# Kernel optimization log

Measured on AMD Instinct MI355X. Metric: run time of the kernel, lower is better.

Reference implementation:

```python
import jax, jax.numpy as jnp
import numpy as np

N_NODES = 50000
N_EDGES = 600000
EMB = 128

def setup_inputs() -> dict:
    key = jax.random.key(0)
    ks = jax.random.split(key, 6)
    h = jax.random.normal(ks[0], (N_NODES, EMB), dtype=jnp.float32)
    edge_attr = jax.random.normal(ks[1], (N_EDGES, EMB), dtype=jnp.float32)
    src = jax.random.randint(ks[2], (N_EDGES,), 0, N_NODES, dtype=jnp.int32)
    dst = jax.random.randint(ks[3], (N_EDGES,), 0, N_NODES, dtype=jnp.int32)
    # MLP: Linear(emb, 2*emb) -> ReLU -> Linear(2*emb, emb)
    W1 = jax.random.normal(ks[4], (EMB, 2 * EMB), dtype=jnp.float32) * (1.0 / np.sqrt(EMB))
    b1 = jnp.zeros((2 * EMB,), dtype=jnp.float32)
    W2 = jax.random.normal(ks[5], (2 * EMB, EMB), dtype=jnp.float32) * (1.0 / np.sqrt(2 * EMB))
    b2 = jnp.zeros((EMB,), dtype=jnp.float32)
    eps = jnp.zeros((1,), dtype=jnp.float32)
    return {"h": h, "edge_attr": edge_attr, "src": src, "dst": dst,
            "W1": W1, "b1": b1, "W2": W2, "b2": b2, "eps": eps}

def reference(h, edge_attr, src, dst, W1, b1, W2, b2, eps):
    # message: m_e = h[src_e] + edge_attr_e   (edge_encoder is None)
    m = h[src] + edge_attr                              # [E, D]
    # reduce: sum messages per destination node
    aggr = jax.ops.segment_sum(m, dst, num_segments=N_NODES)  # [N, D]
    # out = (1 + eps) * h + MLP(aggr)
    hidden = jax.nn.relu(aggr @ W1 + b1)                # [N, 2D]
    mlp_out = hidden @ W2 + b2                          # [N, D]
    return (1.0 + eps) * h + mlp_out
```

## Files before the change

kernel.cpp:

```cpp
#include <hip/hip_runtime.h>

#define N_NODES 50000
#define N_EDGES 600000
#define D 128
#define H2 256
#define TN 16

__global__ __launch_bounds__(256) void hist_kernel(const int* __restrict__ dst,
                                                   int* __restrict__ counts) {
    unsigned int e = blockIdx.x * 256u + threadIdx.x;
    if (e < N_EDGES) atomicAdd(&counts[dst[e]], 1);
}

__global__ __launch_bounds__(256) void scan1_kernel(const int* __restrict__ counts,
                                                    int* __restrict__ scanned,
                                                    int* __restrict__ blocksums) {
    __shared__ int wsum[4];
    const int tid = threadIdx.x;
    const int lane = tid & 63;
    const int wv = tid >> 6;
    const int i = blockIdx.x * 256 + tid;
    const int cval = (i < N_NODES) ? counts[i] : 0;
    int x = cval;
    #pragma unroll
    for (int d = 1; d < 64; d <<= 1) {
        int t = __shfl_up(x, d, 64);
        if (lane >= d) x += t;
    }
    if (lane == 63) wsum[wv] = x;
    __syncthreads();
    if (tid == 0) {
        int s = 0;
        #pragma unroll
        for (int w = 0; w < 4; ++w) { s += wsum[w]; wsum[w] = s; }
    }
    __syncthreads();
    const int prefix = (wv > 0 ? wsum[wv - 1] : 0) + (x - cval);
    if (i < N_NODES) scanned[i] = prefix;
    if (tid == 0) blocksums[blockIdx.x] = wsum[3];
}

__global__ __launch_bounds__(256) void scan2_kernel(const int* __restrict__ blocksums,
                                                    int* __restrict__ blockbase, int nb) {
    __shared__ int wsum[4];
    const int tid = threadIdx.x;
    const int lane = tid & 63;
    const int wv = tid >> 6;
    const int cval = (tid < nb) ? blocksums[tid] : 0;
    int x = cval;
    #pragma unroll
    for (int d = 1; d < 64; d <<= 1) {
        int t = __shfl_up(x, d, 64);
        if (lane >= d) x += t;
    }
    if (lane == 63) wsum[wv] = x;
    __syncthreads();
    if (tid == 0) {
        int s = 0;
        #pragma unroll
        for (int w = 0; w < 4; ++w) { s += wsum[w]; wsum[w] = s; }
    }
    __syncthreads();
    if (tid < nb) blockbase[tid] = (wv > 0 ? wsum[wv - 1] : 0) + (x - cval);
}

__global__ __launch_bounds__(256) void scan3_kernel(const int* __restrict__ scanned,
                                                    const int* __restrict__ blockbase,
                                                    int* __restrict__ offsets,
                                                    int* __restrict__ cursor) {
    const int i = blockIdx.x * 256 + threadIdx.x;
    if (i < N_NODES) {
        const int v = scanned[i] + blockbase[blockIdx.x];
        offsets[i] = v;
        cursor[i] = v;
    }
    if (i == 0) offsets[N_NODES] = N_EDGES;
}

__global__ __launch_bounds__(256) void scatter_kernel(const int* __restrict__ src,
                                                      const int* __restrict__ dst,
                                                      int* __restrict__ cursor,
                                                      int2* __restrict__ perm2) {
    unsigned int e = blockIdx.x * 256u + threadIdx.x;
    if (e >= N_EDGES) return;
    const int d = dst[e];
    const int p = atomicAdd(&cursor[d], 1);
    perm2[p] = make_int2((int)e, src[e]);
}

__global__ __launch_bounds__(256) void fused_kernel(
    const float* __restrict__ h, const float* __restrict__ ea,
    const int* __restrict__ offsets, const int2* __restrict__ perm2,
    const float* __restrict__ W1, const float* __restrict__ b1,
    const float* __restrict__ W2, const float* __restrict__ b2,
    const float* __restrict__ eps, float* __restrict__ out)
{
    __shared__ float s_lds[TN * H2];

    const int tid = threadIdx.x;

    {
        const int t  = tid >> 4;
        const int c8 = (tid & 15) << 3;
        const int node = blockIdx.x * TN + t;
        const int beg = offsets[node];
        const int end = offsets[node + 1];
        float4 a0 = make_float4(0.f, 0.f, 0.f, 0.f);
        float4 a1 = make_float4(0.f, 0.f, 0.f, 0.f);
        if (beg < end) {
            int2 p = perm2[beg];
            for (int j = beg; j < end; ++j) {
                const int2 pn = (j + 1 < end) ? perm2[j + 1] : p;
                const float* er = ea + (size_t)p.x * D + c8;
                const float* hr = h  + (size_t)p.y * D + c8;
                const float4 e0 = *(const float4*)(er);
                const float4 e1 = *(const float4*)(er + 4);
                const float4 h0 = *(const float4*)(hr);
                const float4 h1 = *(const float4*)(hr + 4);
                a0.x += e0.x + h0.x;
                a0.y += e0.y + h0.y;
                a0.z += e0.z + h0.z;
                a0.w += e0.w + h0.w;
                a1.x += e1.x + h1.x;
                a1.y += e1.y + h1.y;
                a1.z += e1.z + h1.z;
                a1.w += e1.w + h1.w;
                p = pn;
            }
        }
        *(float4*)&s_lds[t * D + c8]     = a0;
        *(float4*)&s_lds[t * D + c8 + 4] = a1;
    }
    __syncthreads();

    {
        const int j0 = (tid & 63) << 2;
        const int tbase = (tid >> 6) << 2;
        float4 acc1[4];
        const float4 bv = *(const float4*)(b1 + j0);
        #pragma unroll
        for (int t = 0; t < 4; ++t) acc1[t] = bv;
        for (int k = 0; k < D; k += 4) {
            float4 w[4];
            #pragma unroll
            for (int q = 0; q < 4; ++q)
                w[q] = *(const float4*)(W1 + (size_t)(k + q) * H2 + j0);
            #pragma unroll
            for (int t = 0; t < 4; ++t) {
                const float4 a = *(const float4*)&s_lds[(tbase + t) * D + k];
                acc1[t].x = fmaf(a.x, w[0].x, acc1[t].x);
                acc1[t].y = fmaf(a.x, w[0].y, acc1[t].y);
                acc1[t].z = fmaf(a.x, w[0].z, acc1[t].z);
                acc1[t].w = fmaf(a.x, w[0].w, acc1[t].w);
                acc1[t].x = fmaf(a.y, w[1].x, acc1[t].x);
                acc1[t].y = fmaf(a.y, w[1].y, acc1[t].y);
                acc1[t].z = fmaf(a.y, w[1].z, acc1[t].z);
                acc1[t].w = fmaf(a.y, w[1].w, acc1[t].w);
                acc1[t].x = fmaf(a.z, w[2].x, acc1[t].x);
                acc1[t].y = fmaf(a.z, w[2].y, acc1[t].y);
                acc1[t].z = fmaf(a.z, w[2].z, acc1[t].z);
                acc1[t].w = fmaf(a.z, w[2].w, acc1[t].w);
                acc1[t].x = fmaf(a.w, w[3].x, acc1[t].x);
                acc1[t].y = fmaf(a.w, w[3].y, acc1[t].y);
                acc1[t].z = fmaf(a.w, w[3].z, acc1[t].z);
                acc1[t].w = fmaf(a.w, w[3].w, acc1[t].w);
            }
        }
        __syncthreads();
        #pragma unroll
        for (int t = 0; t < 4; ++t) {
            float4 r;
            r.x = fmaxf(acc1[t].x, 0.f);
            r.y = fmaxf(acc1[t].y, 0.f);
            r.z = fmaxf(acc1[t].z, 0.f);
            r.w = fmaxf(acc1[t].w, 0.f);
            *(float4*)&s_lds[(tbase + t) * H2 + j0] = r;
        }
    }
    __syncthreads();

    {
        const int i0 = (tid & 31) << 2;
        const int g = tid >> 5;
        float4 acc2[2];
        const float4 bv = *(const float4*)(b2 + i0);
        acc2[0] = bv; acc2[1] = bv;
        for (int k = 0; k < H2; k += 4) {
            float4 w[4];
            #pragma unroll
            for (int q = 0; q < 4; ++q)
                w[q] = *(const float4*)(W2 + (size_t)(k + q) * D + i0);
            #pragma unroll
            for (int u = 0; u < 2; ++u) {
                const float4 a = *(const float4*)&s_lds[(g + u * 8) * H2 + k];
                acc2[u].x = fmaf(a.x, w[0].x, acc2[u].x);
                acc2[u].y = fmaf(a.x, w[0].y, acc2[u].y);
                acc2[u].z = fmaf(a.x, w[0].z, acc2[u].z);
                acc2[u].w = fmaf(a.x, w[0].w, acc2[u].w);
                acc2[u].x = fmaf(a.y, w[1].x, acc2[u].x);
                acc2[u].y = fmaf(a.y, w[1].y, acc2[u].y);
                acc2[u].z = fmaf(a.y, w[1].z, acc2[u].z);
                acc2[u].w = fmaf(a.y, w[1].w, acc2[u].w);
                acc2[u].x = fmaf(a.z, w[2].x, acc2[u].x);
                acc2[u].y = fmaf(a.z, w[2].y, acc2[u].y);
                acc2[u].z = fmaf(a.z, w[2].z, acc2[u].z);
                acc2[u].w = fmaf(a.z, w[2].w, acc2[u].w);
                acc2[u].x = fmaf(a.w, w[3].x, acc2[u].x);
                acc2[u].y = fmaf(a.w, w[3].y, acc2[u].y);
                acc2[u].z = fmaf(a.w, w[3].z, acc2[u].z);
                acc2[u].w = fmaf(a.w, w[3].w, acc2[u].w);
            }
        }
        const float ep = 1.0f + eps[0];
        #pragma unroll
        for (int u = 0; u < 2; ++u) {
            const int node = blockIdx.x * TN + g + u * 8;
            const float4 hv = *(const float4*)(h + (size_t)node * D + i0);
            float4 o;
            o.x = fmaf(ep, hv.x, acc2[u].x);
            o.y = fmaf(ep, hv.y, acc2[u].y);
            o.z = fmaf(ep, hv.z, acc2[u].z);
            o.w = fmaf(ep, hv.w, acc2[u].w);
            *(float4*)(out + (size_t)node * D + i0) = o;
        }
    }
}

extern "C" void kernel_launch(void* const* d_in, const int* in_sizes, int n_in,
                              void* d_out, int out_size, void* d_ws, size_t ws_size,
                              hipStream_t stream) {
    const float* h   = (const float*)d_in[0];
    const float* ea  = (const float*)d_in[1];
    const int*   src = (const int*)d_in[2];
    const int*   dst = (const int*)d_in[3];
    const float* W1  = (const float*)d_in[4];
    const float* b1  = (const float*)d_in[5];
    const float* W2  = (const float*)d_in[6];
    const float* b2  = (const float*)d_in[7];
    const float* eps = (const float*)d_in[8];
    float* out = (float*)d_out;

    char* ws = (char*)d_ws;
    int*  counts    = (int*)ws;
    int*  scanned   = (int*)(ws + 256 * 1024);
    int*  offsets   = (int*)(ws + 512 * 1024);
    int*  cursor    = (int*)(ws + 768 * 1024);
    int*  blocksums = (int*)(ws + 1008 * 1024);
    int*  blockbase = (int*)(ws + 1012 * 1024);
    int2* perm2     = (int2*)(ws + 1024 * 1024);

    hipMemsetAsync(counts, 0, N_NODES * sizeof(int), stream);

    const int eblocks = (N_EDGES + 255) / 256;
    const int nblocks = (N_NODES + 255) / 256;

    hist_kernel<<<eblocks, 256, 0, stream>>>(dst, counts);
    scan1_kernel<<<nblocks, 256, 0, stream>>>(counts, scanned, blocksums);
    scan2_kernel<<<1, 256, 0, stream>>>(blocksums, blockbase, nblocks);
    scan3_kernel<<<nblocks, 256, 0, stream>>>(scanned, blockbase, offsets, cursor);
    scatter_kernel<<<eblocks, 256, 0, stream>>>(src, dst, cursor, perm2);
    fused_kernel<<<N_NODES / TN, 256, 0, stream>>>(
        h, ea, offsets, perm2, W1, b1, W2, b2, eps, out);
}
```

Before: 671.0 us.

## Stage edge permutation in LDS, unroll gather by 4, use nontemporal loads

The gather phase now loads each block's slice of the CSR permutation into shared memory in chunks, then has each thread process four edges per iteration with all eight vector loads issued before accumulating, which raises memory-level parallelism over the old one-edge serial chain. Edge-attribute reads and output writes use nontemporal hints so the streamed data does not evict h from cache, and launch bounds ask for four blocks per CU. The cost is extra barriers and an LDS staging pass, plus possible register pressure from the occupancy hint.

```diff
diff --git a/kernel.cpp b/kernel.cpp
--- a/kernel.cpp
+++ b/kernel.cpp
@@ -5,6 +5,16 @@
 #define D 128
 #define H2 256
 #define TN 16
+#define MAXC 2048
+
+typedef float f4 __attribute__((ext_vector_type(4)));
+
+__device__ __forceinline__ f4 ldg_nt(const float* p) {
+    return __builtin_nontemporal_load((const f4*)p);
+}
+__device__ __forceinline__ f4 ldg(const float* p) {
+    return *(const f4*)p;
+}
 
 __global__ __launch_bounds__(256) void hist_kernel(const int* __restrict__ dst,
                                                    int* __restrict__ counts) {
@@ -88,7 +98,7 @@
     perm2[p] = make_int2((int)e, src[e]);
 }
 
-__global__ __launch_bounds__(256) void fused_kernel(
+__global__ __launch_bounds__(256, 4) void fused_kernel(
     const float* __restrict__ h, const float* __restrict__ ea,
     const int* __restrict__ offsets, const int2* __restrict__ perm2,
     const float* __restrict__ W1, const float* __restrict__ b1,
@@ -96,41 +106,59 @@
     const float* __restrict__ eps, float* __restrict__ out)
 {
     __shared__ float s_lds[TN * H2];
+    int2* s_perm = (int2*)s_lds;
 
     const int tid = threadIdx.x;
-
-    {
-        const int t  = tid >> 4;
-        const int c8 = (tid & 15) << 3;
-        const int node = blockIdx.x * TN + t;
-        const int beg = offsets[node];
-        const int end = offsets[node + 1];
-        float4 a0 = make_float4(0.f, 0.f, 0.f, 0.f);
-        float4 a1 = make_float4(0.f, 0.f, 0.f, 0.f);
-        if (beg < end) {
-            int2 p = perm2[beg];
-            for (int j = beg; j < end; ++j) {
-                const int2 pn = (j + 1 < end) ? perm2[j + 1] : p;
-                const float* er = ea + (size_t)p.x * D + c8;
-                const float* hr = h  + (size_t)p.y * D + c8;
-                const float4 e0 = *(const float4*)(er);
-                const float4 e1 = *(const float4*)(er + 4);
-                const float4 h0 = *(const float4*)(hr);
-                const float4 h1 = *(const float4*)(hr + 4);
-                a0.x += e0.x + h0.x;
-                a0.y += e0.y + h0.y;
-                a0.z += e0.z + h0.z;
-                a0.w += e0.w + h0.w;
-                a1.x += e1.x + h1.x;
-                a1.y += e1.y + h1.y;
-                a1.z += e1.z + h1.z;
-                a1.w += e1.w + h1.w;
-                p = pn;
-            }
-        }
-        *(float4*)&s_lds[t * D + c8]     = a0;
-        *(float4*)&s_lds[t * D + c8 + 4] = a1;
-    }
+    const int t  = tid >> 4;
+    const int c8 = (tid & 15) << 3;
+    const int node0 = blockIdx.x * TN;
+    const int blkbeg = offsets[node0];
+    const int blkend = offsets[node0 + TN];
+    const int nbeg = offsets[node0 + t];
+    const int nend = offsets[node0 + t + 1];
+
+    f4 a0 = (f4)(0.f);
+    f4 a1 = (f4)(0.f);
+
+    for (int cb = blkbeg; cb < blkend; cb += MAXC) {
+        const int cnt = min(blkend - cb, MAXC);
+        __syncthreads();
+        for (int i = tid; i < cnt; i += 256) s_perm[i] = perm2[cb + i];
+        __syncthreads();
+        const int lo = max(nbeg - cb, 0);
+        const int hi = min(nend - cb, cnt);
+        int j = lo;
+        for (; j + 3 < hi; j += 4) {
+            int2 p[4];
+            #pragma unroll
+            for (int q = 0; q < 4; ++q) p[q] = s_perm[j + q];
+            f4 ev0[4], ev1[4], hv0[4], hv1[4];
+            #pragma unroll
+            for (int q = 0; q < 4; ++q) {
+                const float* er = ea + (size_t)p[q].x * D + c8;
+                const float* hr = h  + (size_t)p[q].y * D + c8;
+                ev0[q] = ldg_nt(er);
+                ev1[q] = ldg_nt(er + 4);
+                hv0[q] = ldg(hr);
+                hv1[q] = ldg(hr + 4);
+            }
+            #pragma unroll
+            for (int q = 0; q < 4; ++q) {
+                a0 += ev0[q] + hv0[q];
+                a1 += ev1[q] + hv1[q];
+            }
+        }
+        for (; j < hi; ++j) {
+            const int2 p = s_perm[j];
+            const float* er = ea + (size_t)p.x * D + c8;
+            const float* hr = h  + (size_t)p.y * D + c8;
+            a0 += ldg_nt(er)     + ldg(hr);
+            a1 += ldg_nt(er + 4) + ldg(hr + 4);
+        }
+    }
+    __syncthreads();
+    *(f4*)&s_lds[t * D + c8]     = a0;
+    *(f4*)&s_lds[t * D + c8 + 4] = a1;
     __syncthreads();
 
     {
@@ -139,42 +167,42 @@
         float4 acc1[4];
         const float4 bv = *(const float4*)(b1 + j0);
         #pragma unroll
-        for (int t = 0; t < 4; ++t) acc1[t] = bv;
+        for (int q = 0; q < 4; ++q) acc1[q] = bv;
         for (int k = 0; k < D; k += 4) {
             float4 w[4];
             #pragma unroll
             for (int q = 0; q < 4; ++q)
                 w[q] = *(const float4*)(W1 + (size_t)(k + q) * H2 + j0);
             #pragma unroll
-            for (int t = 0; t < 4; ++t) {
-                const float4 a = *(const float4*)&s_lds[(tbase + t) * D + k];
-                acc1[t].x = fmaf(a.x, w[0].x, acc1[t].x);
-                acc1[t].y = fmaf(a.x, w[0].y, acc1[t].y);
-                acc1[t].z = fmaf(a.x, w[0].z, acc1[t].z);
-                acc1[t].w = fmaf(a.x, w[0].w, acc1[t].w);
-                acc1[t].x = fmaf(a.y, w[1].x, acc1[t].x);
-                acc1[t].y = fmaf(a.y, w[1].y, acc1[t].y);
-                acc1[t].z = fmaf(a.y, w[1].z, acc1[t].z);
-                acc1[t].w = fmaf(a.y, w[1].w, acc1[t].w);
-                acc1[t].x = fmaf(a.z, w[2].x, acc1[t].x);
-                acc1[t].y = fmaf(a.z, w[2].y, acc1[t].y);
-                acc1[t].z = fmaf(a.z, w[2].z, acc1[t].z);
-                acc1[t].w = fmaf(a.z, w[2].w, acc1[t].w);
-                acc1[t].x = fmaf(a.w, w[3].x, acc1[t].x);
-                acc1[t].y = fmaf(a.w, w[3].y, acc1[t].y);
-                acc1[t].z = fmaf(a.w, w[3].z, acc1[t].z);
-                acc1[t].w = fmaf(a.w, w[3].w, acc1[t].w);
+            for (int u = 0; u < 4; ++u) {
+                const float4 a = *(const float4*)&s_lds[(tbase + u) * D + k];
+                acc1[u].x = fmaf(a.x, w[0].x, acc1[u].x);
+                acc1[u].y = fmaf(a.x, w[0].y, acc1[u].y);
+                acc1[u].z = fmaf(a.x, w[0].z, acc1[u].z);
+                acc1[u].w = fmaf(a.x, w[0].w, acc1[u].w);
+                acc1[u].x = fmaf(a.y, w[1].x, acc1[u].x);
+                acc1[u].y = fmaf(a.y, w[1].y, acc1[u].y);
+                acc1[u].z = fmaf(a.y, w[1].z, acc1[u].z);
+                acc1[u].w = fmaf(a.y, w[1].w, acc1[u].w);
+                acc1[u].x = fmaf(a.z, w[2].x, acc1[u].x);
+                acc1[u].y = fmaf(a.z, w[2].y, acc1[u].y);
+                acc1[u].z = fmaf(a.z, w[2].z, acc1[u].z);
+                acc1[u].w = fmaf(a.z, w[2].w, acc1[u].w);
+                acc1[u].x = fmaf(a.w, w[3].x, acc1[u].x);
+                acc1[u].y = fmaf(a.w, w[3].y, acc1[u].y);
+                acc1[u].z = fmaf(a.w, w[3].z, acc1[u].z);
+                acc1[u].w = fmaf(a.w, w[3].w, acc1[u].w);
             }
         }
         __syncthreads();
         #pragma unroll
-        for (int t = 0; t < 4; ++t) {
+        for (int u = 0; u < 4; ++u) {
             float4 r;
-            r.x = fmaxf(acc1[t].x, 0.f);
-            r.y = fmaxf(acc1[t].y, 0.f);
-            r.z = fmaxf(acc1[t].z, 0.f);
-            r.w = fmaxf(acc1[t].w, 0.f);
-            *(float4*)&s_lds[(tbase + t) * H2 + j0] = r;
+            r.x = fmaxf(acc1[u].x, 0.f);
+            r.y = fmaxf(acc1[u].y, 0.f);
+            r.z = fmaxf(acc1[u].z, 0.f);
+            r.w = fmaxf(acc1[u].w, 0.f);
+            *(float4*)&s_lds[(tbase + u) * H2 + j0] = r;
         }
     }
     __syncthreads();
@@ -214,14 +242,14 @@
         const float ep = 1.0f + eps[0];
         #pragma unroll
         for (int u = 0; u < 2; ++u) {
-            const int node = blockIdx.x * TN + g + u * 8;
-            const float4 hv = *(const float4*)(h + (size_t)node * D + i0);
-            float4 o;
-            o.x = fmaf(ep, hv.x, acc2[u].x);
-            o.y = fmaf(ep, hv.y, acc2[u].y);
-            o.z = fmaf(ep, hv.z, acc2[u].z);
-            o.w = fmaf(ep, hv.w, acc2[u].w);
-            *(float4*)(out + (size_t)node * D + i0) = o;
+            const int node = node0 + g + u * 8;
+            const f4 hv = ldg(h + (size_t)node * D + i0);
+            f4 o;
+            o[0] = fmaf(ep, hv[0], acc2[u].x);
+            o[1] = fmaf(ep, hv[1], acc2[u].y);
+            o[2] = fmaf(ep, hv[2], acc2[u].z);
+            o[3] = fmaf(ep, hv[3], acc2[u].w);
+            __builtin_nontemporal_store(o, (f4*)(out + (size_t)node * D + i0));
         }
     }
 }
```

Result: faster. 656.4 us (-2.2%).
